# Optimization experiments

Hardware: AMD Instinct MI355X
Metric: run time of the kernel (lower is better)

Reference implementation:

```python
import jax, jax.numpy as jnp
import numpy as np

BS, L, D = 128, 256, 512
H, DK = 2, 256  # heads, head dim
EPS_BN = 1e-5


def _lin(x, W, b):
    # torch Linear: W is (out, in)
    return jnp.einsum('...i,oi->...o', x, W) + b


def _bn(x, g, b, m, v):
    # eval-mode BatchNorm over channel axis = last axis of x
    return (x - m) * (g * jax.lax.rsqrt(v + EPS_BN)) + b


def setup_inputs() -> dict:
    key = jax.random.key(0)
    ks = iter(jax.random.split(key, 64))
    rn = lambda shape, s=0.02: jax.random.normal(next(ks), shape, dtype=jnp.float32) * s
    inp = {}
    inp['cap_emb'] = jax.random.normal(next(ks), (BS, L, D), dtype=jnp.float32)
    inp['lengths'] = jax.random.randint(next(ks), (BS,), 1, L + 1, dtype=jnp.int64 if jax.config.jax_enable_x64 else jnp.int32)
    # GA linears q,k,v
    for nm in ('Wq', 'Wk', 'Wv'):
        inp[nm] = rn((D, D))
    for nm in ('bq', 'bk', 'bv'):
        inp[nm] = rn((D,))
    inp['Wfq'] = rn((DK, DK)); inp['bfq'] = rn((DK,))
    inp['Wfk'] = rn((DK, DK)); inp['bfk'] = rn((DK,))
    inp['Wfg'] = rn((2 * DK, DK)); inp['bfg'] = rn((2 * DK,))
    # BatchNorm params (eval running stats)
    for pre in ('bn1', 'bn2', 'bn3'):
        inp[pre + '_g'] = 1.0 + rn((D,), 0.1)
        inp[pre + '_b'] = rn((D,), 0.1)
        inp[pre + '_m'] = rn((D,), 0.1)
        inp[pre + '_v'] = jax.random.uniform(next(ks), (D,), minval=0.5, maxval=1.5, dtype=jnp.float32)
    # Conv1d weights, torch layout (out, in, k)
    inp['Wc2'] = rn((D, D, 2)); inp['bc2'] = rn((D,))
    inp['Wc3'] = rn((D, D, 3)); inp['bc3'] = rn((D,))
    # MLP 512 -> 1024 -> 512
    inp['Wm1'] = rn((2 * D, D)); inp['bm1'] = rn((2 * D,))
    inp['Wm2'] = rn((D, 2 * D)); inp['bm2'] = rn((D,))
    return inp


def _forward(cap_emb, Wq, bq, Wk, bk, Wv, bv, Wfq, bfq, Wfk, bfk, Wfg, bfg,
             bn1_g, bn1_b, bn1_m, bn1_v, Wc2, bc2, bn2_g, bn2_b, bn2_m, bn2_v,
             Wc3, bc3, bn3_g, bn3_b, bn3_m, bn3_v, Wm1, bm1, Wm2, bm2, lengths):
    bs, seq, dim = cap_emb.shape
    # ---- GA: gated self-attention ----
    def split_heads(x):
        return x.reshape(bs, seq, H, DK).transpose(0, 2, 1, 3)  # [bs,h,seq,dk]
    q = split_heads(_lin(cap_emb, Wq, bq))
    k = split_heads(_lin(cap_emb, Wk, bk))
    v = split_heads(_lin(cap_emb, Wv, bv))
    G = _lin(q, Wfq, bfq) * _lin(k, Wfk, bfk)
    M = jax.nn.sigmoid(_lin(G, Wfg, bfg))  # [bs,h,seq,2*dk]
    qg = q * M[..., :DK]
    kg = k * M[..., DK:]
    # torch.div(..., rounding_mode='floor') == elementwise floor of scaled scores
    scores = jnp.floor(jnp.einsum('bhqd,bhkd->bhqk', qg, kg) / jnp.sqrt(jnp.float32(DK)))
    p_attn = jax.nn.softmax(scores, axis=-1)
    x = jnp.einsum('bhqk,bhkd->bhqd', p_attn, v)
    x = x.transpose(0, 2, 1, 3).reshape(bs, seq, dim)
    # BN over features (eval), dropout is identity in eval mode
    ga_emb = cap_emb + _bn(x, bn1_g, bn1_b, bn1_m, bn1_v)
    # ---- dual conv1d branches ----
    xc = cap_emb.transpose(0, 2, 1)  # [bs, D, L]
    dn = ('NCW', 'OIW', 'NCW')
    c2 = jax.lax.conv_general_dilated(xc, Wc2, window_strides=(2,), padding='VALID', dimension_numbers=dn) + bc2[None, :, None]
    c3 = jax.lax.conv_general_dilated(xc, Wc3, window_strides=(3,), padding='VALID', dimension_numbers=dn) + bc3[None, :, None]
    f2 = jax.nn.relu(_bn(c2.transpose(0, 2, 1), bn2_g, bn2_b, bn2_m, bn2_v))
    f3 = jax.nn.relu(_bn(c3.transpose(0, 2, 1), bn3_g, bn3_b, bn3_m, bn3_v))
    ga_jw = jnp.concatenate([ga_emb, f2, f3], axis=1)
    # ---- residual MLP (dropout identity in eval) ----
    hid = jax.nn.relu(_lin(ga_jw, Wm1, bm1))
    tex_emb = _lin(hid, Wm2, bm2) + ga_jw
    # ---- length-indexed gather ----
    idx = lengths.astype(jnp.int32) - 1
    out = tex_emb[jnp.arange(bs), idx]  # [bs, D]
    # l2norm
    norm = jnp.sqrt(jnp.sum(out * out, axis=-1, keepdims=True)) + 1e-8
    return out / norm


def reference(cap_emb, lengths, Wq, bq, Wk, bk, Wv, bv, Wfq, bfq, Wfk, bfk, Wfg, bfg,
              bn1_g, bn1_b, bn1_m, bn1_v, Wc2, bc2, bn2_g, bn2_b, bn2_m, bn2_v,
              Wc3, bc3, bn3_g, bn3_b, bn3_m, bn3_v, Wm1, bm1, Wm2, bm2):
    return _forward(cap_emb, Wq, bq, Wk, bk, Wv, bv, Wfq, bfq, Wfk, bfk, Wfg, bfg,
                    bn1_g, bn1_b, bn1_m, bn1_v, Wc2, bc2, bn2_g, bn2_b, bn2_m, bn2_v,
                    Wc3, bc3, bn3_g, bn3_b, bn3_m, bn3_v, Wm1, bm1, Wm2, bm2, lengths)
```

## Files before the change

kernel.cpp:

```cpp
#include <hip/hip_runtime.h>
#include <math.h>


typedef short bf16x8 __attribute__((ext_vector_type(8)));
typedef float f32x4 __attribute__((ext_vector_type(4)));
typedef short short4v __attribute__((ext_vector_type(4)));

__device__ __forceinline__ short f2bf(float x) {
    union { float f; unsigned u; } c; c.f = x;
    unsigned r = c.u + 0x7FFFu + ((c.u >> 16) & 1u);
    return (short)(r >> 16);
}
__device__ __forceinline__ float bf2f(short h) {
    union { float f; unsigned u; } c; c.u = ((unsigned)(unsigned short)h) << 16;
    return c.f;
}
__device__ __forceinline__ void glds16(const void* g, void* l) {
    __builtin_amdgcn_global_load_lds(
        (const __attribute__((address_space(1))) void*)g,
        (__attribute__((address_space(3))) void*)l, 16, 0, 0);
}

struct CastArgs {
    const float* src[3];
    short* dst[3];
    int n4[3];
};
__global__ __launch_bounds__(256) void cast_multi(CastArgs a)
{
    const int j = blockIdx.y;
    const float4* s = (const float4*)a.src[j];
    short* d = a.dst[j];
    const int n4 = a.n4[j];
    for (int i = blockIdx.x * 256 + threadIdx.x; i < n4; i += gridDim.x * 256) {
        float4 x = s[i];
        short4v h;
        h.x = f2bf(x.x); h.y = f2bf(x.y); h.z = f2bf(x.z); h.w = f2bf(x.w);
        *(short4v*)&d[i * 4] = h;
    }
}

__global__ __launch_bounds__(256)
void compose2(const float* __restrict__ Wq, const float* __restrict__ bq,
              const float* __restrict__ Wfq, const float* __restrict__ bfq,
              const float* __restrict__ Wk, const float* __restrict__ bk,
              const float* __restrict__ Wfk, const float* __restrict__ bfk,
              short* __restrict__ WaB, float* __restrict__ ba,
              short* __restrict__ WbB, float* __restrict__ bb)
{
    __shared__ float fq[256];
    __shared__ float redc[256];
    const int op = blockIdx.x;
    const int h = op >> 8, o = op & 255;
    const int t = threadIdx.x;
    const bool second = (blockIdx.y == 1);
    const float* W  = second ? Wk  : Wq;
    const float* bv = second ? bk  : bq;
    const float* F  = second ? Wfk : Wfq;
    const float* bf = second ? bfk : bfq;
    short* WB   = second ? WbB : WaB;
    float* bout = second ? bb  : ba;

    fq[t] = F[o * 256 + t];
    redc[t] = fq[t] * bv[h * 256 + t];
    __syncthreads();
    for (int s = 128; s > 0; s >>= 1) {
        if (t < s) redc[t] += redc[t + s];
        __syncthreads();
    }
    if (t == 0) bout[op] = redc[0] + bf[o];
    float s0 = 0.f, s1 = 0.f;
    for (int d = 0; d < 256; ++d) {
        const float f = fq[d];
        const float* wr = W + (size_t)(h * 256 + d) * 512;
        s0 += f * wr[t];
        s1 += f * wr[t + 256];
    }
    const size_t ro = (size_t)op * 512;
    WB[ro + t] = f2bf(s0);
    WB[ro + 256 + t] = f2bf(s1);
}

__device__ __forceinline__ void kloop_1p(
    const short* __restrict__ A, int lda,
    const short* __restrict__ B, int ldb,
    int K, int bm, int bn, short (*lds)[8192], int tid, f32x4 acc[4][4])
{
    const int lane = tid & 63;
    const int wr = (tid >> 7) & 1, wc = (tid >> 6) & 1;
    const int fr = lane & 15, kc = lane >> 4;
    const int r0 = tid >> 2;
    const int e0 = (((tid & 3) ^ ((r0 >> 1) & 3))) * 8;
    const int kce = (kc ^ ((fr >> 1) & 3)) * 8;

    auto stage = [&](int ph, int k0) {
        short* b = lds[ph];
        glds16(A + (size_t)(bm + r0) * lda + k0 + e0,      b + tid * 8);
        glds16(A + (size_t)(bm + r0 + 64) * lda + k0 + e0, b + (tid + 256) * 8);
        glds16(B + (size_t)(bn + r0) * ldb + k0 + e0,      b + 4096 + tid * 8);
        glds16(B + (size_t)(bn + r0 + 64) * ldb + k0 + e0, b + 4096 + (tid + 256) * 8);
    };

    stage(0, 0);
    __syncthreads();
    const int NS = K / 32;
    for (int s = 0; s < NS; ++s) {
        if (s + 1 < NS) stage((s + 1) & 1, (s + 1) * 32);
        const short* b = lds[s & 1];
        bf16x8 ah[4], bh[4];
#pragma unroll
        for (int i = 0; i < 4; ++i)
            ah[i] = *(const bf16x8*)&b[(wr * 64 + i * 16 + fr) * 32 + kce];
#pragma unroll
        for (int i = 0; i < 4; ++i)
            bh[i] = *(const bf16x8*)&b[4096 + (wc * 64 + i * 16 + fr) * 32 + kce];
#pragma unroll
        for (int mi = 0; mi < 4; ++mi)
#pragma unroll
            for (int ni = 0; ni < 4; ++ni)
                acc[mi][ni] = __builtin_amdgcn_mfma_f32_16x16x32_bf16(ah[mi], bh[ni], acc[mi][ni], 0, 0, 0);
        __syncthreads();
    }
}

__global__ __launch_bounds__(256, 2)
void gemm_g(const short* __restrict__ capB,
            const short* __restrict__ WaB, const short* __restrict__ WbB,
            const float* __restrict__ ba, const float* __restrict__ bb,
            short* __restrict__ Gbuf)
{
    __shared__ short lds[2][12288];
    const int tid = threadIdx.x;
    const int bm = blockIdx.y * 128;
    const int bn = blockIdx.x * 128;
    const int z = blockIdx.z;
    const short* B1 = WaB + (size_t)z * 256 * 512;
    const short* B2 = WbB + (size_t)z * 256 * 512;

    const int lane = tid & 63;
    const int wr = (tid >> 7) & 1, wc = (tid >> 6) & 1;
    const int fr = lane & 15, kc = lane >> 4;
    const int r0 = tid >> 2;
    const int e0 = (((tid & 3) ^ ((r0 >> 1) & 3))) * 8;
    const int kce = (kc ^ ((fr >> 1) & 3)) * 8;

    auto stage = [&](int ph, int k0) {
        short* b = lds[ph];
        glds16(capB + (size_t)(bm + r0) * 512 + k0 + e0,      b + tid * 8);
        glds16(capB + (size_t)(bm + r0 + 64) * 512 + k0 + e0, b + (tid + 256) * 8);
        glds16(B1 + (size_t)(bn + r0) * 512 + k0 + e0,        b + 4096 + tid * 8);
        glds16(B1 + (size_t)(bn + r0 + 64) * 512 + k0 + e0,   b + 4096 + (tid + 256) * 8);
        glds16(B2 + (size_t)(bn + r0) * 512 + k0 + e0,        b + 8192 + tid * 8);
        glds16(B2 + (size_t)(bn + r0 + 64) * 512 + k0 + e0,   b + 8192 + (tid + 256) * 8);
    };

    f32x4 acc1[4][4], acc2[4][4];
#pragma unroll
    for (int i = 0; i < 4; ++i)
#pragma unroll
        for (int j = 0; j < 4; ++j) {
            acc1[i][j] = (f32x4){0.f, 0.f, 0.f, 0.f};
            acc2[i][j] = (f32x4){0.f, 0.f, 0.f, 0.f};
        }

    stage(0, 0);
    __syncthreads();
    for (int s = 0; s < 16; ++s) {
        if (s + 1 < 16) stage((s + 1) & 1, (s + 1) * 32);
        const short* b = lds[s & 1];
        bf16x8 ah[4], bh[4];
#pragma unroll
        for (int i = 0; i < 4; ++i)
            ah[i] = *(const bf16x8*)&b[(wr * 64 + i * 16 + fr) * 32 + kce];
#pragma unroll
        for (int i = 0; i < 4; ++i)
            bh[i] = *(const bf16x8*)&b[4096 + (wc * 64 + i * 16 + fr) * 32 + kce];
#pragma unroll
        for (int mi = 0; mi < 4; ++mi)
#pragma unroll
            for (int ni = 0; ni < 4; ++ni)
                acc1[mi][ni] = __builtin_amdgcn_mfma_f32_16x16x32_bf16(ah[mi], bh[ni], acc1[mi][ni], 0, 0, 0);
#pragma unroll
        for (int i = 0; i < 4; ++i)
            bh[i] = *(const bf16x8*)&b[8192 + (wc * 64 + i * 16 + fr) * 32 + kce];
#pragma unroll
        for (int mi = 0; mi < 4; ++mi)
#pragma unroll
            for (int ni = 0; ni < 4; ++ni)
                acc2[mi][ni] = __builtin_amdgcn_mfma_f32_16x16x32_bf16(ah[mi], bh[ni], acc2[mi][ni], 0, 0, 0);
        __syncthreads();
    }

#pragma unroll
    for (int mi = 0; mi < 4; ++mi) {
#pragma unroll
        for (int ni = 0; ni < 4; ++ni) {
#pragma unroll
            for (int r = 0; r < 4; ++r) {
                const int row = bm + wr * 64 + mi * 16 + kc * 4 + r;
                const int col = bn + wc * 64 + ni * 16 + fr;
                const float av  = acc1[mi][ni][r] + ba[z * 256 + col];
                const float lin = acc2[mi][ni][r] + bb[z * 256 + col];
                Gbuf[(size_t)row * 512 + z * 256 + col] = f2bf(lin * av);
            }
        }
    }
}

__global__ __launch_bounds__(256, 2)
void gemm_kg(const short* __restrict__ Gbuf,
             const short* __restrict__ Wfg2B, const float* __restrict__ bias,
             const short* __restrict__ capB,
             const short* __restrict__ WkB, const float* __restrict__ bk,
             const float* __restrict__ qg, float* __restrict__ scorep)
{
    __shared__ short lds[2][8192];
    __shared__ float sp[256];
    const int tid = threadIdx.x;
    const int bm = blockIdx.y * 128;
    const int bn = blockIdx.x * 128;
    const int z = blockIdx.z;

    f32x4 acc1[4][4], acc2[4][4];
#pragma unroll
    for (int i = 0; i < 4; ++i)
#pragma unroll
        for (int j = 0; j < 4; ++j) {
            acc1[i][j] = (f32x4){0.f, 0.f, 0.f, 0.f};
            acc2[i][j] = (f32x4){0.f, 0.f, 0.f, 0.f};
        }

    kloop_1p(Gbuf + (size_t)z * 256, 512, Wfg2B, 256, 256, bm, bn, lds, tid, acc1);
    kloop_1p(capB, 512, WkB + (size_t)z * 256 * 512, 512, 512, bm, bn, lds, tid, acc2);

    const int lane = tid & 63;
    const int wr = (tid >> 7) & 1, wc = (tid >> 6) & 1;
    const int fr = lane & 15, kc = lane >> 4;

    float qgv[4];
    float pt[4][4];
    {
        const int b = bm >> 8;
#pragma unroll
        for (int ni = 0; ni < 4; ++ni)
            qgv[ni] = qg[b * 512 + z * 256 + bn + wc * 64 + ni * 16 + fr];
#pragma unroll
        for (int mi = 0; mi < 4; ++mi)
#pragma unroll
            for (int r = 0; r < 4; ++r) pt[mi][r] = 0.f;
    }

#pragma unroll
    for (int mi = 0; mi < 4; ++mi) {
#pragma unroll
        for (int ni = 0; ni < 4; ++ni) {
#pragma unroll
            for (int r = 0; r < 4; ++r) {
                const int col = bn + wc * 64 + ni * 16 + fr;
                const float v = acc1[mi][ni][r] + bias[col];
                const float e = acc2[mi][ni][r] + bk[z * 256 + col];
                const float kgv = e / (1.f + expf(-v));
                pt[mi][r] += kgv * qgv[ni];
            }
        }
    }

#pragma unroll
    for (int mi = 0; mi < 4; ++mi) {
#pragma unroll
        for (int r = 0; r < 4; ++r) {
            float p = pt[mi][r];
            p += __shfl_xor(p, 1);
            p += __shfl_xor(p, 2);
            p += __shfl_xor(p, 4);
            p += __shfl_xor(p, 8);
            if (fr == 0) {
                const int row_local = wr * 64 + mi * 16 + kc * 4 + r;
                sp[row_local * 2 + wc] = p;
            }
        }
    }
    __syncthreads();
    if (tid < 128) {
        const int row = bm + tid;
        const float s = sp[tid * 2] + sp[tid * 2 + 1];
        const int b = row >> 8, j = row & 255;
        scorep[((size_t)(b * 2 + z) * 256 + j) * 2 + blockIdx.x] = s;
    }
}

__global__ __launch_bounds__(256)
void qg_kernel(const float* __restrict__ cap,
               const short* __restrict__ Gbuf,
               const float* __restrict__ Wq, const float* __restrict__ bq,
               const float* __restrict__ Wfg, const float* __restrict__ bfg,
               const int* __restrict__ lengths, float* __restrict__ qg)
{
    __shared__ float cr[512];
    __shared__ float gs[256];
    const int b = blockIdx.x >> 1, h = blockIdx.x & 1;
    const int t = threadIdx.x;
    int r = lengths[b] - 1;
    if (r < 0) r = 0;
    if (r > 255) r = 255;
    const size_t base = ((size_t)b * 256 + r) * 512;
    cr[t] = cap[base + t];
    cr[t + 256] = cap[base + 256 + t];
    gs[t] = bf2f(Gbuf[base + h * 256 + t]);
    __syncthreads();
    const float4* wq4 = (const float4*)(Wq + (size_t)(h * 256 + t) * 512);
    float q = 0.f;
    for (int k4 = 0; k4 < 128; ++k4) {
        float4 w = wq4[k4];
        q += w.x * cr[k4 * 4 + 0] + w.y * cr[k4 * 4 + 1]
           + w.z * cr[k4 * 4 + 2] + w.w * cr[k4 * 4 + 3];
    }
    q += bq[h * 256 + t];
    const float4* w4 = (const float4*)(Wfg + (size_t)t * 256);
    float a = 0.f;
    for (int k4 = 0; k4 < 64; ++k4) {
        float4 w = w4[k4];
        a += w.x * gs[k4 * 4 + 0] + w.y * gs[k4 * 4 + 1]
           + w.z * gs[k4 * 4 + 2] + w.w * gs[k4 * 4 + 3];
    }
    a += bfg[t];
    qg[b * 512 + h * 256 + t] = q / (1.f + expf(-a));
}

__global__ __launch_bounds__(256)
void pbar_kernel(const float* __restrict__ scorep, const short* __restrict__ capB,
                 float* __restrict__ pbar)
{
    __shared__ float sc[512], red[512];
    const int b = blockIdx.y, cg = blockIdx.x;
    const int t = threadIdx.x;
#pragma unroll
    for (int i = 0; i < 2; ++i) {
        const int o = t + i * 256;
        const int h = o >> 8, j = o & 255;
        const size_t si = ((size_t)(b * 2 + h) * 256 + j) * 2;
        sc[o] = floorf((scorep[si] + scorep[si + 1]) * 0.0625f);
    }
    __syncthreads();
    red[t] = sc[t]; red[t + 256] = sc[t + 256];
    __syncthreads();
    for (int s = 128; s > 0; s >>= 1) {
        if (t < s) {
            red[t] = fmaxf(red[t], red[t + s]);
            red[256 + t] = fmaxf(red[256 + t], red[256 + t + s]);
        }
        __syncthreads();
    }
    const float mx0 = red[0], mx1 = red[256];
    __syncthreads();
    const float e0 = expf(sc[t] - mx0);
    const float e1 = expf(sc[t + 256] - mx1);
    red[t] = e0; red[t + 256] = e1;
    __syncthreads();
    for (int s = 128; s > 0; s >>= 1) {
        if (t < s) { red[t] += red[t + s]; red[256 + t] += red[256 + t + s]; }
        __syncthreads();
    }
    sc[t] = e0 / red[0];
    sc[t + 256] = e1 / red[256];
    __syncthreads();

    const int c = cg * 64 + (t & 63);
    const int jg = t >> 6;
    float a0 = 0.f, a1 = 0.f;
    for (int j = jg * 64; j < jg * 64 + 64; ++j) {
        const float cv = bf2f(capB[((size_t)(b * 256 + j)) * 512 + c]);
        a0 += sc[j] * cv;
        a1 += sc[256 + j] * cv;
    }
    red[t] = a0;
    __syncthreads();
    if (t < 64) {
        const float s0 = red[t] + red[t + 64] + red[t + 128] + red[t + 192];
        pbar[b * 1024 + cg * 64 + t] = s0;
    }
    __syncthreads();
    red[t] = a1;
    __syncthreads();
    if (t < 64) {
        const float s1 = red[t] + red[t + 64] + red[t + 128] + red[t + 192];
        pbar[b * 1024 + 512 + cg * 64 + t] = s1;
    }
}

__global__ __launch_bounds__(256)
void bnx_kernel(const float* __restrict__ pbar, const float* __restrict__ cap,
                const int* __restrict__ lengths,
                const float* __restrict__ Wv, const float* __restrict__ bv,
                const float* __restrict__ g1, const float* __restrict__ b1,
                const float* __restrict__ m1, const float* __restrict__ v1,
                float* __restrict__ xga)
{
    __shared__ float pb[1024];
    const int b = blockIdx.x;
    const int t = threadIdx.x;
    int r = lengths[b] - 1;
    if (r < 0) r = 0;
    if (r > 255) r = 255;
    const size_t base = ((size_t)b * 256 + r) * 512;
    pb[t] = pbar[b * 1024 + t];
    pb[t + 256] = pbar[b * 1024 + 256 + t];
    pb[t + 512] = pbar[b * 1024 + 512 + t];
    pb[t + 768] = pbar[b * 1024 + 768 + t];
    __syncthreads();
    float x0 = 0.f, x1 = 0.f;
    {
        const float4* w4 = (const float4*)(Wv + (size_t)t * 512);
        for (int k4 = 0; k4 < 128; ++k4) {
            float4 w = w4[k4];
            x0 += w.x * pb[k4 * 4 + 0] + w.y * pb[k4 * 4 + 1]
                + w.z * pb[k4 * 4 + 2] + w.w * pb[k4 * 4 + 3];
        }
        x0 += bv[t];
    }
    {
        const float4* w4 = (const float4*)(Wv + (size_t)(t + 256) * 512);
        for (int k4 = 0; k4 < 128; ++k4) {
            float4 w = w4[k4];
            x1 += w.x * pb[512 + k4 * 4 + 0] + w.y * pb[512 + k4 * 4 + 1]
                + w.z * pb[512 + k4 * 4 + 2] + w.w * pb[512 + k4 * 4 + 3];
        }
        x1 += bv[t + 256];
    }
    const int c0 = t, c1 = t + 256;
    const float s0 = g1[c0] / sqrtf(v1[c0] + 1e-5f);
    const float s1 = g1[c1] / sqrtf(v1[c1] + 1e-5f);
    xga[b * 512 + c0] = cap[base + c0] + (x0 - m1[c0]) * s0 + b1[c0];
    xga[b * 512 + c1] = cap[base + c1] + (x1 - m1[c1]) * s1 + b1[c1];
}

__global__ __launch_bounds__(256)
void mlp1(const float* __restrict__ xga, const float* __restrict__ W,
          const float* __restrict__ bias, float* __restrict__ hid)
{
    __shared__ float xs[16 * 512];
    const int r0 = blockIdx.y * 16;
    const int c0 = blockIdx.x * 64;
    for (int i = threadIdx.x; i < 2048; i += 256)
        ((float4*)xs)[i] = ((const float4*)(xga + (size_t)r0 * 512))[i];
    __syncthreads();
    const int col = c0 + (threadIdx.x & 63);
    const int rg = (threadIdx.x >> 6) * 4;
    float acc[4] = {0.f, 0.f, 0.f, 0.f};
    const float4* w4 = (const float4*)(W + (size_t)col * 512);
    for (int k4 = 0; k4 < 128; ++k4) {
        float4 w = w4[k4];
#pragma unroll
        for (int rr = 0; rr < 4; ++rr) {
            float4 x = *(const float4*)&xs[(rg + rr) * 512 + k4 * 4];
            acc[rr] += w.x * x.x + w.y * x.y + w.z * x.z + w.w * x.w;
        }
    }
    const float bb = bias[col];
#pragma unroll
    for (int rr = 0; rr < 4; ++rr)
        hid[(size_t)(r0 + rg + rr) * 1024 + col] = fmaxf(acc[rr] + bb, 0.f);
}

__global__ __launch_bounds__(256)
void mlp2(const float* __restrict__ hid, const float* __restrict__ W,
          const float* __restrict__ bias, const float* __restrict__ xga,
          float* __restrict__ tex)
{
    __shared__ float xs[16 * 1024];
    const int r0 = blockIdx.y * 16;
    const int c0 = blockIdx.x * 64;
    for (int i = threadIdx.x; i < 4096; i += 256)
        ((float4*)xs)[i] = ((const float4*)(hid + (size_t)r0 * 1024))[i];
    __syncthreads();
    const int col = c0 + (threadIdx.x & 63);
    const int rg = (threadIdx.x >> 6) * 4;
    float acc[4] = {0.f, 0.f, 0.f, 0.f};
    const float4* w4 = (const float4*)(W + (size_t)col * 1024);
    for (int k4 = 0; k4 < 256; ++k4) {
        float4 w = w4[k4];
#pragma unroll
        for (int rr = 0; rr < 4; ++rr) {
            float4 x = *(const float4*)&xs[(rg + rr) * 1024 + k4 * 4];
            acc[rr] += w.x * x.x + w.y * x.y + w.z * x.z + w.w * x.w;
        }
    }
    const float bb = bias[col];
#pragma unroll
    for (int rr = 0; rr < 4; ++rr) {
        const int row = r0 + rg + rr;
        tex[(size_t)row * 512 + col] = acc[rr] + bb + xga[(size_t)row * 512 + col];
    }
}

__global__ __launch_bounds__(256)
void norm_out(const float* __restrict__ tex, float* __restrict__ out)
{
    __shared__ float red[256];
    const int b = blockIdx.x;
    const int t = threadIdx.x;
    const float a = tex[b * 512 + t];
    const float c = tex[b * 512 + 256 + t];
    red[t] = a * a + c * c;
    __syncthreads();
    for (int s = 128; s > 0; s >>= 1) {
        if (t < s) red[t] += red[t + s];
        __syncthreads();
    }
    const float inv = 1.f / (sqrtf(red[0]) + 1e-8f);
    out[b * 512 + t] = a * inv;
    out[b * 512 + 256 + t] = c * inv;
}

extern "C" void kernel_launch(void* const* d_in, const int* in_sizes, int n_in,
                              void* d_out, int out_size, void* d_ws, size_t ws_size,
                              hipStream_t stream)
{
    const float* cap = (const float*)d_in[0];
    const int* lengths = (const int*)d_in[1];
    const float* Wq  = (const float*)d_in[2];
    const float* Wk  = (const float*)d_in[3];
    const float* Wv  = (const float*)d_in[4];
    const float* bq  = (const float*)d_in[5];
    const float* bk  = (const float*)d_in[6];
    const float* bv  = (const float*)d_in[7];
    const float* Wfq = (const float*)d_in[8];
    const float* bfq = (const float*)d_in[9];
    const float* Wfk = (const float*)d_in[10];
    const float* bfk = (const float*)d_in[11];
    const float* Wfg = (const float*)d_in[12];
    const float* bfg = (const float*)d_in[13];
    const float* g1  = (const float*)d_in[14];
    const float* b1  = (const float*)d_in[15];
    const float* m1  = (const float*)d_in[16];
    const float* v1  = (const float*)d_in[17];
    const float* Wm1 = (const float*)d_in[30];
    const float* bm1 = (const float*)d_in[31];
    const float* Wm2 = (const float*)d_in[32];
    const float* bm2 = (const float*)d_in[33];
    float* out = (float*)d_out;

    char* w = (char*)d_ws;
    const size_t MB = 1024 * 1024;
    short* capB = (short*)(w);
    short* Gbuf = (short*)(w + 32 * MB);
    char* wp = w + 64 * MB;
    short* WkB   = (short*)wp; wp += 524288;
    short* WaB   = (short*)wp; wp += 524288;
    short* WbB   = (short*)wp; wp += 524288;
    short* Wfg2B = (short*)wp; wp += 131072;
    float* ba     = (float*)wp; wp += 2048;
    float* bb     = (float*)wp; wp += 2048;
    float* qg     = (float*)wp; wp += 262144;
    float* scorep = (float*)wp; wp += 524288;
    float* pbar   = (float*)wp; wp += 524288;
    float* xga    = (float*)wp; wp += 262144;
    float* hid    = (float*)wp; wp += 524288;
    float* tex    = (float*)wp; wp += 262144;

    CastArgs ca;
    ca.src[0] = cap;          ca.dst[0] = capB;  ca.n4[0] = 4194304;
    ca.src[1] = Wk;           ca.dst[1] = WkB;   ca.n4[1] = 65536;
    ca.src[2] = Wfg + 65536;  ca.dst[2] = Wfg2B; ca.n4[2] = 16384;
    cast_multi<<<dim3(4096, 3), 256, 0, stream>>>(ca);

    compose2<<<dim3(512, 2), 256, 0, stream>>>(Wq, bq, Wfq, bfq, Wk, bk, Wfk, bfk,
                                               WaB, ba, WbB, bb);

    gemm_g<<<dim3(2, 256, 2), 256, 0, stream>>>(capB, WaB, WbB, ba, bb, Gbuf);

    qg_kernel<<<dim3(256), 256, 0, stream>>>(cap, Gbuf, Wq, bq, Wfg, bfg, lengths, qg);

    gemm_kg<<<dim3(2, 256, 2), 256, 0, stream>>>(Gbuf, Wfg2B, bfg + 256,
                                                 capB, WkB, bk, qg, scorep);

    pbar_kernel<<<dim3(8, 128), 256, 0, stream>>>(scorep, capB, pbar);
    bnx_kernel<<<dim3(128), 256, 0, stream>>>(pbar, cap, lengths, Wv, bv, g1, b1, m1, v1, xga);

    mlp1<<<dim3(16, 8), 256, 0, stream>>>(xga, Wm1, bm1, hid);
    mlp2<<<dim3(8, 8), 256, 0, stream>>>(hid, Wm2, bm2, xga, tex);
    norm_out<<<dim3(128), 256, 0, stream>>>(tex, out);
}
```

Before: 269.9 us.

## Widen GEMM tiles to full 256 columns with 512-thread blocks

gemm_g and gemm_kg now use 128x256 output tiles covering the whole head width. Each block has 8 waves in a 2x4 layout instead of two blocks per row tile each doing 128 columns. The A tile (capB or Gbuf rows) is loaded once per block instead of twice, and gemm_kg's row-score partials are reduced inside the block. scorep shrinks to one value per row and pbar_kernel no longer sums two halves. In exchange the blocks use more LDS and there are half as many, which changes occupancy and latency hiding.

```diff
diff --git a/kernel.cpp b/kernel.cpp
--- a/kernel.cpp
+++ b/kernel.cpp
@@ -81,13 +81,14 @@
     WB[ro + 256 + t] = f2bf(s1);
 }
 
-__device__ __forceinline__ void kloop_1p(
+__device__ __forceinline__ void kloop_w(
     const short* __restrict__ A, int lda,
     const short* __restrict__ B, int ldb,
-    int K, int bm, int bn, short (*lds)[8192], int tid, f32x4 acc[4][4])
+    int K, int bm, short (*lds)[12288], int tid, f32x4 acc[4][4])
 {
     const int lane = tid & 63;
-    const int wr = (tid >> 7) & 1, wc = (tid >> 6) & 1;
+    const int wv = tid >> 6;
+    const int wr = wv >> 2, wc = wv & 3;
     const int fr = lane & 15, kc = lane >> 4;
     const int r0 = tid >> 2;
     const int e0 = (((tid & 3) ^ ((r0 >> 1) & 3))) * 8;
@@ -95,10 +96,9 @@
 
     auto stage = [&](int ph, int k0) {
         short* b = lds[ph];
-        glds16(A + (size_t)(bm + r0) * lda + k0 + e0,      b + tid * 8);
-        glds16(A + (size_t)(bm + r0 + 64) * lda + k0 + e0, b + (tid + 256) * 8);
-        glds16(B + (size_t)(bn + r0) * ldb + k0 + e0,      b + 4096 + tid * 8);
-        glds16(B + (size_t)(bn + r0 + 64) * ldb + k0 + e0, b + 4096 + (tid + 256) * 8);
+        glds16(A + (size_t)(bm + r0) * lda + k0 + e0,    b + r0 * 32 + (tid & 3) * 8);
+        glds16(B + (size_t)r0 * ldb + k0 + e0,           b + 4096 + r0 * 32 + (tid & 3) * 8);
+        glds16(B + (size_t)(r0 + 128) * ldb + k0 + e0,   b + 4096 + (r0 + 128) * 32 + (tid & 3) * 8);
     };
 
     stage(0, 0);
@@ -123,22 +123,22 @@
     }
 }
 
-__global__ __launch_bounds__(256, 2)
+__global__ __launch_bounds__(512)
 void gemm_g(const short* __restrict__ capB,
             const short* __restrict__ WaB, const short* __restrict__ WbB,
             const float* __restrict__ ba, const float* __restrict__ bb,
             short* __restrict__ Gbuf)
 {
-    __shared__ short lds[2][12288];
+    __shared__ short lds[2][20480];
     const int tid = threadIdx.x;
-    const int bm = blockIdx.y * 128;
-    const int bn = blockIdx.x * 128;
-    const int z = blockIdx.z;
+    const int bm = blockIdx.x * 128;
+    const int z = blockIdx.y;
     const short* B1 = WaB + (size_t)z * 256 * 512;
     const short* B2 = WbB + (size_t)z * 256 * 512;
 
     const int lane = tid & 63;
-    const int wr = (tid >> 7) & 1, wc = (tid >> 6) & 1;
+    const int wv = tid >> 6;
+    const int wr = wv >> 2, wc = wv & 3;
     const int fr = lane & 15, kc = lane >> 4;
     const int r0 = tid >> 2;
     const int e0 = (((tid & 3) ^ ((r0 >> 1) & 3))) * 8;
@@ -146,12 +146,11 @@
 
     auto stage = [&](int ph, int k0) {
         short* b = lds[ph];
-        glds16(capB + (size_t)(bm + r0) * 512 + k0 + e0,      b + tid * 8);
-        glds16(capB + (size_t)(bm + r0 + 64) * 512 + k0 + e0, b + (tid + 256) * 8);
-        glds16(B1 + (size_t)(bn + r0) * 512 + k0 + e0,        b + 4096 + tid * 8);
-        glds16(B1 + (size_t)(bn + r0 + 64) * 512 + k0 + e0,   b + 4096 + (tid + 256) * 8);
-        glds16(B2 + (size_t)(bn + r0) * 512 + k0 + e0,        b + 8192 + tid * 8);
-        glds16(B2 + (size_t)(bn + r0 + 64) * 512 + k0 + e0,   b + 8192 + (tid + 256) * 8);
+        glds16(capB + (size_t)(bm + r0) * 512 + k0 + e0, b + r0 * 32 + (tid & 3) * 8);
+        glds16(B1 + (size_t)r0 * 512 + k0 + e0,          b + 4096 + r0 * 32 + (tid & 3) * 8);
+        glds16(B1 + (size_t)(r0 + 128) * 512 + k0 + e0,  b + 4096 + (r0 + 128) * 32 + (tid & 3) * 8);
+        glds16(B2 + (size_t)r0 * 512 + k0 + e0,          b + 12288 + r0 * 32 + (tid & 3) * 8);
+        glds16(B2 + (size_t)(r0 + 128) * 512 + k0 + e0,  b + 12288 + (r0 + 128) * 32 + (tid & 3) * 8);
     };
 
     f32x4 acc1[4][4], acc2[4][4];
@@ -182,7 +181,7 @@
                 acc1[mi][ni] = __builtin_amdgcn_mfma_f32_16x16x32_bf16(ah[mi], bh[ni], acc1[mi][ni], 0, 0, 0);
 #pragma unroll
         for (int i = 0; i < 4; ++i)
-            bh[i] = *(const bf16x8*)&b[8192 + (wc * 64 + i * 16 + fr) * 32 + kce];
+            bh[i] = *(const bf16x8*)&b[12288 + (wc * 64 + i * 16 + fr) * 32 + kce];
 #pragma unroll
         for (int mi = 0; mi < 4; ++mi)
 #pragma unroll
@@ -198,7 +197,7 @@
 #pragma unroll
             for (int r = 0; r < 4; ++r) {
                 const int row = bm + wr * 64 + mi * 16 + kc * 4 + r;
-                const int col = bn + wc * 64 + ni * 16 + fr;
+                const int col = wc * 64 + ni * 16 + fr;
                 const float av  = acc1[mi][ni][r] + ba[z * 256 + col];
                 const float lin = acc2[mi][ni][r] + bb[z * 256 + col];
                 Gbuf[(size_t)row * 512 + z * 256 + col] = f2bf(lin * av);
@@ -207,19 +206,18 @@
     }
 }
 
-__global__ __launch_bounds__(256, 2)
+__global__ __launch_bounds__(512)
 void gemm_kg(const short* __restrict__ Gbuf,
              const short* __restrict__ Wfg2B, const float* __restrict__ bias,
              const short* __restrict__ capB,
              const short* __restrict__ WkB, const float* __restrict__ bk,
              const float* __restrict__ qg, float* __restrict__ scorep)
 {
-    __shared__ short lds[2][8192];
-    __shared__ float sp[256];
+    __shared__ short lds[2][12288];
+    __shared__ float sp[128][4];
     const int tid = threadIdx.x;
-    const int bm = blockIdx.y * 128;
-    const int bn = blockIdx.x * 128;
-    const int z = blockIdx.z;
+    const int bm = blockIdx.x * 128;
+    const int z = blockIdx.y;
 
     f32x4 acc1[4][4], acc2[4][4];
 #pragma unroll
@@ -230,11 +228,12 @@
             acc2[i][j] = (f32x4){0.f, 0.f, 0.f, 0.f};
         }
 
-    kloop_1p(Gbuf + (size_t)z * 256, 512, Wfg2B, 256, 256, bm, bn, lds, tid, acc1);
-    kloop_1p(capB, 512, WkB + (size_t)z * 256 * 512, 512, 512, bm, bn, lds, tid, acc2);
+    kloop_w(Gbuf + (size_t)z * 256, 512, Wfg2B, 256, 256, bm, lds, tid, acc1);
+    kloop_w(capB, 512, WkB + (size_t)z * 256 * 512, 512, 512, bm, lds, tid, acc2);
 
     const int lane = tid & 63;
-    const int wr = (tid >> 7) & 1, wc = (tid >> 6) & 1;
+    const int wv = tid >> 6;
+    const int wr = wv >> 2, wc = wv & 3;
     const int fr = lane & 15, kc = lane >> 4;
 
     float qgv[4];
@@ -243,7 +242,7 @@
         const int b = bm >> 8;
 #pragma unroll
         for (int ni = 0; ni < 4; ++ni)
-            qgv[ni] = qg[b * 512 + z * 256 + bn + wc * 64 + ni * 16 + fr];
+            qgv[ni] = qg[b * 512 + z * 256 + wc * 64 + ni * 16 + fr];
 #pragma unroll
         for (int mi = 0; mi < 4; ++mi)
 #pragma unroll
@@ -256,7 +255,7 @@
         for (int ni = 0; ni < 4; ++ni) {
 #pragma unroll
             for (int r = 0; r < 4; ++r) {
-                const int col = bn + wc * 64 + ni * 16 + fr;
+                const int col = wc * 64 + ni * 16 + fr;
                 const float v = acc1[mi][ni][r] + bias[col];
                 const float e = acc2[mi][ni][r] + bk[z * 256 + col];
                 const float kgv = e / (1.f + expf(-v));
@@ -276,16 +275,16 @@
             p += __shfl_xor(p, 8);
             if (fr == 0) {
                 const int row_local = wr * 64 + mi * 16 + kc * 4 + r;
-                sp[row_local * 2 + wc] = p;
+                sp[row_local][wc] = p;
             }
         }
     }
     __syncthreads();
     if (tid < 128) {
+        const float s = sp[tid][0] + sp[tid][1] + sp[tid][2] + sp[tid][3];
         const int row = bm + tid;
-        const float s = sp[tid * 2] + sp[tid * 2 + 1];
         const int b = row >> 8, j = row & 255;
-        scorep[((size_t)(b * 2 + z) * 256 + j) * 2 + blockIdx.x] = s;
+        scorep[(size_t)b * 512 + z * 256 + j] = s;
     }
 }
 
@@ -337,9 +336,7 @@
 #pragma unroll
     for (int i = 0; i < 2; ++i) {
         const int o = t + i * 256;
-        const int h = o >> 8, j = o & 255;
-        const size_t si = ((size_t)(b * 2 + h) * 256 + j) * 2;
-        sc[o] = floorf((scorep[si] + scorep[si + 1]) * 0.0625f);
+        sc[o] = floorf(scorep[(size_t)b * 512 + o] * 0.0625f);
     }
     __syncthreads();
     red[t] = sc[t]; red[t + 256] = sc[t + 256];
@@ -552,7 +549,7 @@
     float* ba     = (float*)wp; wp += 2048;
     float* bb     = (float*)wp; wp += 2048;
     float* qg     = (float*)wp; wp += 262144;
-    float* scorep = (float*)wp; wp += 524288;
+    float* scorep = (float*)wp; wp += 262144;
     float* pbar   = (float*)wp; wp += 524288;
     float* xga    = (float*)wp; wp += 262144;
     float* hid    = (float*)wp; wp += 524288;
@@ -567,12 +564,12 @@
     compose2<<<dim3(512, 2), 256, 0, stream>>>(Wq, bq, Wfq, bfq, Wk, bk, Wfk, bfk,
                                                WaB, ba, WbB, bb);
 
-    gemm_g<<<dim3(2, 256, 2), 256, 0, stream>>>(capB, WaB, WbB, ba, bb, Gbuf);
+    gemm_g<<<dim3(256, 2), 512, 0, stream>>>(capB, WaB, WbB, ba, bb, Gbuf);
 
     qg_kernel<<<dim3(256), 256, 0, stream>>>(cap, Gbuf, Wq, bq, Wfg, bfg, lengths, qg);
 
-    gemm_kg<<<dim3(2, 256, 2), 256, 0, stream>>>(Gbuf, Wfg2B, bfg + 256,
-                                                 capB, WkB, bk, qg, scorep);
+    gemm_kg<<<dim3(256, 2), 512, 0, stream>>>(Gbuf, Wfg2B, bfg + 256,
+                                              capB, WkB, bk, qg, scorep);
 
     pbar_kernel<<<dim3(8, 128), 256, 0, stream>>>(scorep, capB, pbar);
     bnx_kernel<<<dim3(128), 256, 0, stream>>>(pbar, cap, lengths, Wv, bv, g1, b1, m1, v1, xga);
```

Measured after the change: 271.2 us. About the same (+0.5%).
